# Optimization experiments

Measured on AMD Instinct MI355X. Metric: run time of the kernel, lower is better.

## Reference

```python
import jax, jax.numpy as jnp
import numpy as np

W = 4  # kernel_size

def setup_inputs() -> dict:
    key = jax.random.key(0)
    k1, k2, k3, k4 = jax.random.split(key, 4)
    B, T, D, H = 4, 4096, 2048, 256
    x = jax.random.normal(k1, (B, T, D), dtype=jnp.float32)
    # stored as [in, out] (transpose of torch Linear convention)
    w1 = jax.random.normal(k2, (D, H), dtype=jnp.float32) * 0.02
    w2 = jax.random.normal(k3, (H, D * W), dtype=jnp.float32) * 0.02
    b2 = jax.random.normal(k4, (D * W,), dtype=jnp.float32) * 0.02
    return {"x": x, "w1": w1, "w2": w2, "b2": b2}

def reference(x, w1, w2, b2):
    # x: [B, T, D]
    B, T, D = x.shape
    # kernel generator: Linear -> silu -> Linear(+bias)
    h = jax.nn.silu(jnp.einsum('btd,dh->bth', x, w1))
    flat = jnp.einsum('bth,ho->bto', h, w2) + b2          # [B, T, D*W]
    kernels = flat.reshape(B, T, D, W)                    # per-token depthwise kernels
    # causal depthwise dynamic conv: out[t] = sum_w k[t, :, w] * x[t - (W-1) + w]
    xp = jnp.pad(x, ((0, 0), (W - 1, 0), (0, 0)))         # left-pad time by W-1
    out = jnp.zeros_like(x)
    for w in range(W):  # W is a small static constant (4)
        out = out + kernels[..., w] * xp[:, w:w + T, :]
    return jax.nn.silu(out)
```

## Files before the change

### kernel.cpp

```cpp
#include <hip/hip_runtime.h>

typedef unsigned short u16;
typedef unsigned int   u32;
typedef __attribute__((ext_vector_type(8))) short short8;
typedef __attribute__((ext_vector_type(4))) float floatx4;

#define T_DIM 4096
#define D_DIM 2048
#define H_DIM 256
#define M_DIM 16384
#define NFLAT 8192

__device__ __forceinline__ u16 f2bf(float f) {
  union { float f; u32 u; } c; c.f = f;
  u32 x = c.u;
  x += 0x7FFFu + ((x >> 16) & 1u);
  return (u16)(x >> 16);
}
__device__ __forceinline__ u32 pk2(float a, float b) {
  return (u32)f2bf(a) | ((u32)f2bf(b) << 16);
}

__device__ __forceinline__ void glds16(const void* g, void* l) {
  __builtin_amdgcn_global_load_lds(
      (const __attribute__((address_space(1))) void*)g,
      (__attribute__((address_space(3))) void*)l, 16, 0, 0);
}

__global__ void __launch_bounds__(256) tr_cvt(const float* __restrict__ src,
                                              u16* __restrict__ dst, int R, int C) {
  __shared__ u16 tile[32][33];
  const int tx = threadIdx.x & 31;
  const int ty = threadIdx.x >> 5;
  const int c0 = blockIdx.x * 32;
  const int r0 = blockIdx.y * 32;
  #pragma unroll
  for (int i = ty; i < 32; i += 8)
    tile[i][tx] = f2bf(src[(size_t)(r0 + i) * C + (c0 + tx)]);
  __syncthreads();
  #pragma unroll
  for (int i = ty; i < 32; i += 8)
    dst[(size_t)(c0 + i) * R + (r0 + tx)] = tile[tx][i];
}

__global__ void __launch_bounds__(256) gemm1_silu(const float* __restrict__ X,
                                                  const u16* __restrict__ Bt,
                                                  u16* __restrict__ H) {
  __shared__ __align__(16) u16 As[64][64];
  __shared__ __align__(16) u16 Bs[128][64];
  const int tid  = threadIdx.x;
  const int lane = tid & 63, l15 = lane & 15, quad = lane >> 4;
  const int wv   = tid >> 6, wy = wv >> 1, wx = wv & 1;
  const int m0   = blockIdx.y * 64;
  const int n0   = blockIdx.x * 128;
  const int srow = lane >> 3, sc = lane & 7;

  floatx4 acc[2][4];
  const floatx4 zf = {0.f, 0.f, 0.f, 0.f};
  #pragma unroll
  for (int i = 0; i < 2; ++i)
    #pragma unroll
    for (int j = 0; j < 4; ++j) acc[i][j] = zf;

  float4 fA[2][2];
  #pragma unroll
  for (int i = 0; i < 2; ++i) {
    int s = i * 256 + tid, row = s >> 3, g = s & 7;
    const float* xs = &X[(size_t)(m0 + row) * D_DIM + g * 8];
    fA[i][0] = *(const float4*)xs;
    fA[i][1] = *(const float4*)(xs + 4);
  }

  for (int k0 = 0; k0 < D_DIM; k0 += 64) {
    __syncthreads();
    #pragma unroll
    for (int i = 0; i < 2; ++i) {
      int s = i * 256 + tid, row = s >> 3, g = s & 7, c = g ^ (row & 7);
      uint4 pk;
      pk.x = pk2(fA[i][0].x, fA[i][0].y);
      pk.y = pk2(fA[i][0].z, fA[i][0].w);
      pk.z = pk2(fA[i][1].x, fA[i][1].y);
      pk.w = pk2(fA[i][1].z, fA[i][1].w);
      *(uint4*)&As[row][c * 8] = pk;
    }
    #pragma unroll
    for (int ci = 0; ci < 4; ++ci) {
      int ch  = ci * 4 + wv;
      int row = ch * 8 + srow;
      glds16(&Bt[(size_t)(n0 + row) * D_DIM + k0 + (sc ^ (row & 7)) * 8],
             (char*)Bs + ch * 1024);
    }
    __syncthreads();
    {
      int kn = (k0 + 64 < D_DIM) ? (k0 + 64) : 0;
      #pragma unroll
      for (int i = 0; i < 2; ++i) {
        int s = i * 256 + tid, row = s >> 3, g = s & 7;
        const float* xs = &X[(size_t)(m0 + row) * D_DIM + kn + g * 8];
        fA[i][0] = *(const float4*)xs;
        fA[i][1] = *(const float4*)(xs + 4);
      }
    }
    short8 af[2][2], bfr[4][2];
    #pragma unroll
    for (int ks = 0; ks < 2; ++ks) {
      #pragma unroll
      for (int mi = 0; mi < 2; ++mi) {
        int row = wy * 32 + mi * 16 + l15;
        af[mi][ks] = *(const short8*)&As[row][((ks * 4 + quad) ^ (row & 7)) * 8];
      }
      #pragma unroll
      for (int ni = 0; ni < 4; ++ni) {
        int row = wx * 64 + ni * 16 + l15;
        bfr[ni][ks] = *(const short8*)&Bs[row][((ks * 4 + quad) ^ (row & 7)) * 8];
      }
    }
    #pragma unroll
    for (int ks = 0; ks < 2; ++ks)
      #pragma unroll
      for (int mi = 0; mi < 2; ++mi)
        #pragma unroll
        for (int ni = 0; ni < 4; ++ni)
          acc[mi][ni] = __builtin_amdgcn_mfma_f32_16x16x32_bf16(af[mi][ks], bfr[ni][ks], acc[mi][ni], 0, 0, 0);
  }
  #pragma unroll
  for (int mi = 0; mi < 2; ++mi)
    #pragma unroll
    for (int ni = 0; ni < 4; ++ni)
      #pragma unroll
      for (int r = 0; r < 4; ++r) {
        float v = acc[mi][ni][r];
        v = v / (1.f + __expf(-v));
        int row = m0 + wy * 32 + mi * 16 + quad * 4 + r;
        int col = n0 + wx * 64 + ni * 16 + l15;
        H[(size_t)row * H_DIM + col] = f2bf(v);
      }
}

__global__ void __launch_bounds__(256) gemm2_conv_silu(const u16* __restrict__ Hin,
                                                       const u16* __restrict__ Bt,
                                                       const float* __restrict__ bias,
                                                       const float* __restrict__ X,
                                                       float* __restrict__ Out) {
  __shared__ __align__(16) u16 As[128][64];
  __shared__ __align__(16) u16 Bs[128][64];
  const int tid  = threadIdx.x;
  const int lane = tid & 63, l15 = lane & 15, quad = lane >> 4;
  const int wv   = tid >> 6, wy = wv >> 1, wx = wv & 1;
  const int m0   = blockIdx.y * 128;
  const int d0   = blockIdx.x * 32;
  const int srow = lane >> 3, sc = lane & 7;

  floatx4 acc[4][4];
  const floatx4 zf = {0.f, 0.f, 0.f, 0.f};
  #pragma unroll
  for (int i = 0; i < 4; ++i)
    #pragma unroll
    for (int j = 0; j < 4; ++j) acc[i][j] = zf;

  for (int k0 = 0; k0 < H_DIM; k0 += 64) {
    __syncthreads();
    #pragma unroll
    for (int ci = 0; ci < 4; ++ci) {
      int ch  = ci * 4 + wv;
      int row = ch * 8 + srow;
      int g   = (sc ^ (row & 7)) * 8;
      glds16(&Hin[(size_t)(m0 + row) * H_DIM + k0 + g], (char*)As + ch * 1024);
      int fc = (d0 + ((row >> 6) << 4) + (row & 15)) * 4 + ((row >> 4) & 3);
      glds16(&Bt[(size_t)fc * H_DIM + k0 + g], (char*)Bs + ch * 1024);
    }
    __syncthreads();
    short8 af[4][2], bfr[4][2];
    #pragma unroll
    for (int ks = 0; ks < 2; ++ks) {
      #pragma unroll
      for (int mi = 0; mi < 4; ++mi) {
        int row = wy * 64 + mi * 16 + l15;
        af[mi][ks] = *(const short8*)&As[row][((ks * 4 + quad) ^ (row & 7)) * 8];
      }
      #pragma unroll
      for (int ni = 0; ni < 4; ++ni) {
        int row = wx * 64 + ni * 16 + l15;
        bfr[ni][ks] = *(const short8*)&Bs[row][((ks * 4 + quad) ^ (row & 7)) * 8];
      }
    }
    #pragma unroll
    for (int ks = 0; ks < 2; ++ks)
      #pragma unroll
      for (int mi = 0; mi < 4; ++mi)
        #pragma unroll
        for (int ni = 0; ni < 4; ++ni)
          acc[mi][ni] = __builtin_amdgcn_mfma_f32_16x16x32_bf16(af[mi][ks], bfr[ni][ks], acc[mi][ni], 0, 0, 0);
  }

  const int d     = d0 + wx * 16 + l15;
  const float4 bv = *(const float4*)&bias[(size_t)d * 4];
  const int tbase = m0 & (T_DIM - 1);
  const int bbase = m0 - tbase;
  const float* xcol = &X[(size_t)bbase * D_DIM + d];
  float* ocol       = &Out[(size_t)m0 * D_DIM + d];

  #pragma unroll
  for (int mi = 0; mi < 4; ++mi) {
    int t0 = wy * 64 + mi * 16 + quad * 4;
    int tq = tbase + t0;
    float xv[7];
    #pragma unroll
    for (int j = 0; j < 7; ++j) {
      int tt = tq - 3 + j;
      xv[j] = (tt >= 0) ? xcol[(size_t)tt * D_DIM] : 0.f;
    }
    #pragma unroll
    for (int r = 0; r < 4; ++r) {
      float c0 = acc[mi][0][r] + bv.x;
      float c1 = acc[mi][1][r] + bv.y;
      float c2 = acc[mi][2][r] + bv.z;
      float c3 = acc[mi][3][r] + bv.w;
      float o  = c0 * xv[r] + c1 * xv[r + 1] + c2 * xv[r + 2] + c3 * xv[r + 3];
      float y  = o / (1.f + __expf(-o));
      ocol[(size_t)(t0 + r) * D_DIM] = y;
    }
  }
}

extern "C" void kernel_launch(void* const* d_in, const int* in_sizes, int n_in,
                              void* d_out, int out_size, void* d_ws, size_t ws_size,
                              hipStream_t stream) {
  const float* x  = (const float*)d_in[0];
  const float* w1 = (const float*)d_in[1];
  const float* w2 = (const float*)d_in[2];
  const float* b2 = (const float*)d_in[3];
  float* out = (float*)d_out;

  u16* w1t = (u16*)d_ws;
  u16* w2t = w1t + (size_t)H_DIM * D_DIM;
  u16* h   = w2t + (size_t)NFLAT * H_DIM;

  tr_cvt<<<dim3(H_DIM / 32, D_DIM / 32), 256, 0, stream>>>(w1, w1t, D_DIM, H_DIM);
  tr_cvt<<<dim3(NFLAT / 32, H_DIM / 32), 256, 0, stream>>>(w2, w2t, H_DIM, NFLAT);
  gemm1_silu<<<dim3(2, M_DIM / 64), 256, 0, stream>>>(x, w1t, h);
  gemm2_conv_silu<<<dim3(D_DIM / 32, M_DIM / 128), 256, 0, stream>>>(h, w2t, b2, x, out);
}
```

Baseline: 342.1 us.

## Double-buffer LDS tiles in both GEMMs and merge weight transpose launches

Both GEMM kernels now use two LDS buffers per operand. The next k-tile is staged (global_load_lds for B/H, bf16-packed registers for X) while MFMAs run on the current tile, which leaves one barrier per iteration instead of two. The two weight transpose/convert kernels are also merged into a single launch to save one kernel launch. In exchange the kernels use twice as much shared memory, which may lower occupancy, and gemm2 has only four k-steps, so there is little to overlap there.

```diff
diff --git a/kernel.cpp b/kernel.cpp
--- a/kernel.cpp
+++ b/kernel.cpp
@@ -27,13 +27,23 @@
       (__attribute__((address_space(3))) void*)l, 16, 0, 0);
 }
 
-__global__ void __launch_bounds__(256) tr_cvt(const float* __restrict__ src,
-                                              u16* __restrict__ dst, int R, int C) {
+__global__ void __launch_bounds__(256) tr_cvt_all(const float* __restrict__ w1,
+                                                  u16* __restrict__ w1t,
+                                                  const float* __restrict__ w2,
+                                                  u16* __restrict__ w2t) {
   __shared__ u16 tile[32][33];
+  int bid = blockIdx.x;
+  const float* src; u16* dst; int R, C, c0, r0;
+  if (bid < 512) {
+    src = w1; dst = w1t; R = D_DIM; C = H_DIM;
+    c0 = (bid & 7) * 32; r0 = (bid >> 3) * 32;
+  } else {
+    int b = bid - 512;
+    src = w2; dst = w2t; R = H_DIM; C = NFLAT;
+    c0 = (b & 255) * 32; r0 = (b >> 8) * 32;
+  }
   const int tx = threadIdx.x & 31;
   const int ty = threadIdx.x >> 5;
-  const int c0 = blockIdx.x * 32;
-  const int r0 = blockIdx.y * 32;
   #pragma unroll
   for (int i = ty; i < 32; i += 8)
     tile[i][tx] = f2bf(src[(size_t)(r0 + i) * C + (c0 + tx)]);
@@ -46,8 +56,8 @@
 __global__ void __launch_bounds__(256) gemm1_silu(const float* __restrict__ X,
                                                   const u16* __restrict__ Bt,
                                                   u16* __restrict__ H) {
-  __shared__ __align__(16) u16 As[64][64];
-  __shared__ __align__(16) u16 Bs[128][64];
+  __shared__ __align__(16) u16 As[2][64][64];
+  __shared__ __align__(16) u16 Bs[2][128][64];
   const int tid  = threadIdx.x;
   const int lane = tid & 63, l15 = lane & 15, quad = lane >> 4;
   const int wv   = tid >> 6, wy = wv >> 1, wx = wv & 1;
@@ -63,56 +73,63 @@
     for (int j = 0; j < 4; ++j) acc[i][j] = zf;
 
   float4 fA[2][2];
-  #pragma unroll
-  for (int i = 0; i < 2; ++i) {
-    int s = i * 256 + tid, row = s >> 3, g = s & 7;
-    const float* xs = &X[(size_t)(m0 + row) * D_DIM + g * 8];
-    fA[i][0] = *(const float4*)xs;
-    fA[i][1] = *(const float4*)(xs + 4);
-  }
-
-  for (int k0 = 0; k0 < D_DIM; k0 += 64) {
-    __syncthreads();
-    #pragma unroll
-    for (int i = 0; i < 2; ++i) {
-      int s = i * 256 + tid, row = s >> 3, g = s & 7, c = g ^ (row & 7);
-      uint4 pk;
-      pk.x = pk2(fA[i][0].x, fA[i][0].y);
-      pk.y = pk2(fA[i][0].z, fA[i][0].w);
-      pk.z = pk2(fA[i][1].x, fA[i][1].y);
-      pk.w = pk2(fA[i][1].z, fA[i][1].w);
-      *(uint4*)&As[row][c * 8] = pk;
-    }
-    #pragma unroll
-    for (int ci = 0; ci < 4; ++ci) {
-      int ch  = ci * 4 + wv;
-      int row = ch * 8 + srow;
-      glds16(&Bt[(size_t)(n0 + row) * D_DIM + k0 + (sc ^ (row & 7)) * 8],
-             (char*)Bs + ch * 1024);
-    }
-    __syncthreads();
-    {
-      int kn = (k0 + 64 < D_DIM) ? (k0 + 64) : 0;
-      #pragma unroll
-      for (int i = 0; i < 2; ++i) {
-        int s = i * 256 + tid, row = s >> 3, g = s & 7;
-        const float* xs = &X[(size_t)(m0 + row) * D_DIM + kn + g * 8];
-        fA[i][0] = *(const float4*)xs;
-        fA[i][1] = *(const float4*)(xs + 4);
-      }
-    }
+
+#define G1_LOADA(KT)                                                          \
+  _Pragma("unroll")                                                           \
+  for (int i = 0; i < 2; ++i) {                                               \
+    int s = i * 256 + tid, row = s >> 3, g = s & 7;                           \
+    const float* xs = &X[(size_t)(m0 + row) * D_DIM + (KT) * 64 + g * 8];     \
+    fA[i][0] = *(const float4*)xs;                                            \
+    fA[i][1] = *(const float4*)(xs + 4);                                      \
+  }
+
+#define G1_WRITEA(BUF)                                                        \
+  _Pragma("unroll")                                                           \
+  for (int i = 0; i < 2; ++i) {                                               \
+    int s = i * 256 + tid, row = s >> 3, g = s & 7, c = g ^ (row & 7);        \
+    uint4 pk;                                                                 \
+    pk.x = pk2(fA[i][0].x, fA[i][0].y);                                       \
+    pk.y = pk2(fA[i][0].z, fA[i][0].w);                                       \
+    pk.z = pk2(fA[i][1].x, fA[i][1].y);                                       \
+    pk.w = pk2(fA[i][1].z, fA[i][1].w);                                       \
+    *(uint4*)&As[BUF][row][c * 8] = pk;                                       \
+  }
+
+#define G1_STAGEB(KT, BUF)                                                    \
+  _Pragma("unroll")                                                           \
+  for (int ci = 0; ci < 4; ++ci) {                                            \
+    int ch  = ci * 4 + wv;                                                    \
+    int row = ch * 8 + srow;                                                  \
+    glds16(&Bt[(size_t)(n0 + row) * D_DIM + (KT) * 64 + (sc ^ (row & 7)) * 8],\
+           (char*)Bs + (BUF) * 16384 + ch * 1024);                            \
+  }
+
+  G1_LOADA(0);
+  G1_STAGEB(0, 0);
+  G1_WRITEA(0);
+  G1_LOADA(1);
+  __syncthreads();
+
+  #pragma unroll 2
+  for (int t = 0; t < 32; ++t) {
+    const int b = t & 1;
+    if (t + 1 < 32) {
+      G1_WRITEA(b ^ 1);
+      G1_STAGEB(t + 1, b ^ 1);
+    }
+    if (t + 2 < 32) G1_LOADA(t + 2);
     short8 af[2][2], bfr[4][2];
     #pragma unroll
     for (int ks = 0; ks < 2; ++ks) {
       #pragma unroll
       for (int mi = 0; mi < 2; ++mi) {
         int row = wy * 32 + mi * 16 + l15;
-        af[mi][ks] = *(const short8*)&As[row][((ks * 4 + quad) ^ (row & 7)) * 8];
+        af[mi][ks] = *(const short8*)&As[b][row][((ks * 4 + quad) ^ (row & 7)) * 8];
       }
       #pragma unroll
       for (int ni = 0; ni < 4; ++ni) {
         int row = wx * 64 + ni * 16 + l15;
-        bfr[ni][ks] = *(const short8*)&Bs[row][((ks * 4 + quad) ^ (row & 7)) * 8];
+        bfr[ni][ks] = *(const short8*)&Bs[b][row][((ks * 4 + quad) ^ (row & 7)) * 8];
       }
     }
     #pragma unroll
@@ -122,7 +139,9 @@
         #pragma unroll
         for (int ni = 0; ni < 4; ++ni)
           acc[mi][ni] = __builtin_amdgcn_mfma_f32_16x16x32_bf16(af[mi][ks], bfr[ni][ks], acc[mi][ni], 0, 0, 0);
-  }
+    if (t + 1 < 32) __syncthreads();
+  }
+
   #pragma unroll
   for (int mi = 0; mi < 2; ++mi)
     #pragma unroll
@@ -135,6 +154,9 @@
         int col = n0 + wx * 64 + ni * 16 + l15;
         H[(size_t)row * H_DIM + col] = f2bf(v);
       }
+#undef G1_LOADA
+#undef G1_WRITEA
+#undef G1_STAGEB
 }
 
 __global__ void __launch_bounds__(256) gemm2_conv_silu(const u16* __restrict__ Hin,
@@ -142,8 +164,8 @@
                                                        const float* __restrict__ bias,
                                                        const float* __restrict__ X,
                                                        float* __restrict__ Out) {
-  __shared__ __align__(16) u16 As[128][64];
-  __shared__ __align__(16) u16 Bs[128][64];
+  __shared__ __align__(16) u16 As[2][128][64];
+  __shared__ __align__(16) u16 Bs[2][128][64];
   const int tid  = threadIdx.x;
   const int lane = tid & 63, l15 = lane & 15, quad = lane >> 4;
   const int wv   = tid >> 6, wy = wv >> 1, wx = wv & 1;
@@ -158,30 +180,38 @@
     #pragma unroll
     for (int j = 0; j < 4; ++j) acc[i][j] = zf;
 
-  for (int k0 = 0; k0 < H_DIM; k0 += 64) {
-    __syncthreads();
-    #pragma unroll
-    for (int ci = 0; ci < 4; ++ci) {
-      int ch  = ci * 4 + wv;
-      int row = ch * 8 + srow;
-      int g   = (sc ^ (row & 7)) * 8;
-      glds16(&Hin[(size_t)(m0 + row) * H_DIM + k0 + g], (char*)As + ch * 1024);
-      int fc = (d0 + ((row >> 6) << 4) + (row & 15)) * 4 + ((row >> 4) & 3);
-      glds16(&Bt[(size_t)fc * H_DIM + k0 + g], (char*)Bs + ch * 1024);
-    }
-    __syncthreads();
+#define G2_STAGE(KT, BUF)                                                     \
+  _Pragma("unroll")                                                           \
+  for (int ci = 0; ci < 4; ++ci) {                                            \
+    int ch  = ci * 4 + wv;                                                    \
+    int row = ch * 8 + srow;                                                  \
+    int g   = (sc ^ (row & 7)) * 8;                                           \
+    glds16(&Hin[(size_t)(m0 + row) * H_DIM + (KT) * 64 + g],                  \
+           (char*)As + (BUF) * 16384 + ch * 1024);                            \
+    int fc = (d0 + ((row >> 6) << 4) + (row & 15)) * 4 + ((row >> 4) & 3);    \
+    glds16(&Bt[(size_t)fc * H_DIM + (KT) * 64 + g],                           \
+           (char*)Bs + (BUF) * 16384 + ch * 1024);                            \
+  }
+
+  G2_STAGE(0, 0);
+  __syncthreads();
+
+  #pragma unroll
+  for (int t = 0; t < 4; ++t) {
+    const int b = t & 1;
+    if (t + 1 < 4) G2_STAGE(t + 1, b ^ 1);
     short8 af[4][2], bfr[4][2];
     #pragma unroll
     for (int ks = 0; ks < 2; ++ks) {
       #pragma unroll
       for (int mi = 0; mi < 4; ++mi) {
         int row = wy * 64 + mi * 16 + l15;
-        af[mi][ks] = *(const short8*)&As[row][((ks * 4 + quad) ^ (row & 7)) * 8];
+        af[mi][ks] = *(const short8*)&As[b][row][((ks * 4 + quad) ^ (row & 7)) * 8];
       }
       #pragma unroll
       for (int ni = 0; ni < 4; ++ni) {
         int row = wx * 64 + ni * 16 + l15;
-        bfr[ni][ks] = *(const short8*)&Bs[row][((ks * 4 + quad) ^ (row & 7)) * 8];
+        bfr[ni][ks] = *(const short8*)&Bs[b][row][((ks * 4 + quad) ^ (row & 7)) * 8];
       }
     }
     #pragma unroll
@@ -191,7 +221,9 @@
         #pragma unroll
         for (int ni = 0; ni < 4; ++ni)
           acc[mi][ni] = __builtin_amdgcn_mfma_f32_16x16x32_bf16(af[mi][ks], bfr[ni][ks], acc[mi][ni], 0, 0, 0);
-  }
+    if (t + 1 < 4) __syncthreads();
+  }
+#undef G2_STAGE
 
   const int d     = d0 + wx * 16 + l15;
   const float4 bv = *(const float4*)&bias[(size_t)d * 4];
@@ -236,8 +268,7 @@
   u16* w2t = w1t + (size_t)H_DIM * D_DIM;
   u16* h   = w2t + (size_t)NFLAT * H_DIM;
 
-  tr_cvt<<<dim3(H_DIM / 32, D_DIM / 32), 256, 0, stream>>>(w1, w1t, D_DIM, H_DIM);
-  tr_cvt<<<dim3(NFLAT / 32, H_DIM / 32), 256, 0, stream>>>(w2, w2t, H_DIM, NFLAT);
+  tr_cvt_all<<<512 + 2048, 256, 0, stream>>>(w1, w1t, w2, w2t);
   gemm1_silu<<<dim3(2, M_DIM / 64), 256, 0, stream>>>(x, w1t, h);
   gemm2_conv_silu<<<dim3(D_DIM / 32, M_DIM / 128), 256, 0, stream>>>(h, w2t, b2, x, out);
 }
```

Measured after the change: 369.0 us. 7.9% more time.
